# Kernel tuning notes

Hardware: AMD Instinct MI355X
Metric: run time of the kernel (lower is better)

Reference implementation:

```python
import jax, jax.numpy as jnp
import numpy as np

N_NODES = 100000
N_EDGES = 3200000
F_IN = 256
HEADS = 8
C_OUT = 8
NEG_SLOPE = 0.2


def setup_inputs() -> dict:
    key = jax.random.key(0)
    k1, k2, k3, k4, k5, k6 = jax.random.split(key, 6)
    x = jax.random.normal(k1, (N_NODES, F_IN), dtype=jnp.float32)
    edge_index = jax.random.randint(k2, (2, N_EDGES), 0, N_NODES, dtype=jnp.int64)
    W = jax.random.normal(k3, (F_IN, HEADS * C_OUT), dtype=jnp.float32) * (1.0 / np.sqrt(F_IN))
    att_src = jax.random.normal(k4, (HEADS, C_OUT), dtype=jnp.float32) * 0.1
    att_dst = jax.random.normal(k5, (HEADS, C_OUT), dtype=jnp.float32) * 0.1
    bias = jax.random.normal(k6, (HEADS * C_OUT,), dtype=jnp.float32) * 0.01
    return {"x": x, "edge_index": edge_index, "W": W, "att_src": att_src, "att_dst": att_dst, "bias": bias}


def reference(x, edge_index, W, att_src, att_dst, bias):
    # GATConv (PyG semantics), concat=True, inference (dropout off).
    N = x.shape[0]
    H, C = att_src.shape
    h = (x @ W).reshape(N, H, C)                      # [N,H,C] transformed features
    a_src = jnp.einsum('nhc,hc->nh', h, att_src)      # [N,H]
    a_dst = jnp.einsum('nhc,hc->nh', h, att_dst)      # [N,H]
    src, dst = edge_index[0], edge_index[1]
    # per-edge raw attention logits
    e = jax.nn.leaky_relu(a_src[src] + a_dst[dst], NEG_SLOPE)  # [E,H]
    # segment softmax over incoming edges of each destination node
    m = jax.ops.segment_max(e, dst, num_segments=N)            # [N,H]
    e = jnp.exp(e - m[dst])
    s = jax.ops.segment_sum(e, dst, num_segments=N)            # [N,H]
    alpha = e / (s[dst] + 1e-16)                               # [E,H]
    # scatter-add weighted neighbor features
    out = jax.ops.segment_sum(alpha[:, :, None] * h[src], dst, num_segments=N)  # [N,H,C]
    return out.reshape(N, H * C) + bias
```

## Files before the change

### kernel.cpp

```cpp
#include <hip/hip_runtime.h>
#include <hip/hip_fp16.h>
#include <math.h>

#define F_IN 256
#define HC 64
#define NHEAD 8
#define NEG 0.2f
#define BSH 7
#define BSZ 128
#define CAP 5376
#define HCAP 2944

typedef __attribute__((ext_vector_type(8))) short bf16x8;
typedef __attribute__((ext_vector_type(4))) float f32x4;

union BV { uint4 q; bf16x8 v; };

__device__ __forceinline__ unsigned int hi_pair(float a, float b) {
  return __builtin_amdgcn_perm(__float_as_uint(a), __float_as_uint(b), 0x03020706u);
}
__device__ __forceinline__ unsigned int lo_pair(float a, float b) {
  float ra = a - __uint_as_float(__float_as_uint(a) & 0xffff0000u);
  float rb = b - __uint_as_float(__float_as_uint(b) & 0xffff0000u);
  return __builtin_amdgcn_perm(__float_as_uint(ra), __float_as_uint(rb), 0x03020706u);
}

__global__ __launch_bounds__(256) void k_prep(const float* __restrict__ W,
                                              unsigned short* __restrict__ Wp,
                                              int* __restrict__ bcursor, int NB) {
  int b = blockIdx.x, t = threadIdx.x;
  if (b >= 64) {
    int i = (b - 64) * 256 + t;
    if (i < NB) bcursor[i] = 0;
    return;
  }
  int idx = b * 256 + t;
  int k = idx >> 6, c = idx & 63;
  float w = W[idx];
  unsigned int u = __float_as_uint(w);
  unsigned short hi = (unsigned short)((u + 0x7fffu + ((u >> 16) & 1u)) >> 16);
  float r = w - __uint_as_float((unsigned int)hi << 16);
  unsigned int ur = __float_as_uint(r);
  unsigned short lo = (unsigned short)((ur + 0x7fffu + ((ur >> 16) & 1u)) >> 16);
  int ks = k >> 5, j = k & 7, lg = (k >> 3) & 3;
  int lane = lg * 16 + (c & 15), cg = c >> 4;
  int off = ((ks * 4 + cg) * 64 + lane) * 8 + j;
  Wp[off] = hi;
  Wp[16384 + off] = lo;
}

__global__ __launch_bounds__(512, 4) void k_fused(
    const float* __restrict__ x, const uint4* __restrict__ Wp4,
    const float* __restrict__ att_src, const float* __restrict__ att_dst,
    __half2* __restrict__ h2, float* __restrict__ asrc, float* __restrict__ adst,
    const int* __restrict__ edge, int* __restrict__ bcursor,
    unsigned int* __restrict__ entries, int N, int E, int NB, int NG, int NP) {
  __shared__ unsigned long long srt8[8192];
  __shared__ int hist[1024];
  __shared__ int loff[1024];
  __shared__ int basearr[1024];
  __shared__ int pr[512];
  int b = blockIdx.x;
  int mn = min(NG, NP), m2 = 2 * mn;
  int type, idx;
  if (b < m2) { type = b & 1; idx = b >> 1; }
  else { type = (NG > NP) ? 0 : 1; idx = mn + (b - m2); }
  int t = threadIdx.x;

  if (type == 0) {
    int wv = t >> 6, l = t & 63;
    int lr = l & 15, lg = l >> 4;
    int r0 = idx * 256 + wv * 32;
    int ra = r0 + lr;      if (ra > N - 1) ra = N - 1;
    int rb = r0 + 16 + lr; if (rb > N - 1) rb = N - 1;
    const float* xr0 = x + (size_t)ra * F_IN + lg * 8;
    const float* xr1 = x + (size_t)rb * F_IN + lg * 8;
    const uint4* wp = Wp4 + l;

    float as4[4], ad4[4];
#pragma unroll
    for (int cg = 0; cg < 4; cg++) {
      as4[cg] = att_src[cg * 16 + lr];
      ad4[cg] = att_dst[cg * 16 + lr];
    }

    f32x4 acc[2][4];
#pragma unroll
    for (int i = 0; i < 2; i++)
#pragma unroll
      for (int j = 0; j < 4; j++) acc[i][j] = (f32x4){0.f, 0.f, 0.f, 0.f};

#pragma unroll
    for (int ks = 0; ks < 8; ks++) {
      float4 p0 = *(const float4*)(xr0 + ks * 32);
      float4 q0 = *(const float4*)(xr0 + ks * 32 + 4);
      float4 p1 = *(const float4*)(xr1 + ks * 32);
      float4 q1 = *(const float4*)(xr1 + ks * 32 + 4);
      BV bh[4], bl[4];
#pragma unroll
      for (int cg = 0; cg < 4; cg++) {
        bh[cg].q = wp[(ks * 4 + cg) * 64];
        bl[cg].q = wp[2048 + (ks * 4 + cg) * 64];
      }
      BV ah0, al0, ah1, al1;
      ah0.q.x = hi_pair(p0.x, p0.y); ah0.q.y = hi_pair(p0.z, p0.w);
      ah0.q.z = hi_pair(q0.x, q0.y); ah0.q.w = hi_pair(q0.z, q0.w);
      al0.q.x = lo_pair(p0.x, p0.y); al0.q.y = lo_pair(p0.z, p0.w);
      al0.q.z = lo_pair(q0.x, q0.y); al0.q.w = lo_pair(q0.z, q0.w);
      ah1.q.x = hi_pair(p1.x, p1.y); ah1.q.y = hi_pair(p1.z, p1.w);
      ah1.q.z = hi_pair(q1.x, q1.y); ah1.q.w = hi_pair(q1.z, q1.w);
      al1.q.x = lo_pair(p1.x, p1.y); al1.q.y = lo_pair(p1.z, p1.w);
      al1.q.z = lo_pair(q1.x, q1.y); al1.q.w = lo_pair(q1.z, q1.w);
#pragma unroll
      for (int cg = 0; cg < 4; cg++) {
        acc[0][cg] = __builtin_amdgcn_mfma_f32_16x16x32_bf16(ah0.v, bh[cg].v, acc[0][cg], 0, 0, 0);
        acc[0][cg] = __builtin_amdgcn_mfma_f32_16x16x32_bf16(al0.v, bh[cg].v, acc[0][cg], 0, 0, 0);
        acc[0][cg] = __builtin_amdgcn_mfma_f32_16x16x32_bf16(ah0.v, bl[cg].v, acc[0][cg], 0, 0, 0);
        acc[1][cg] = __builtin_amdgcn_mfma_f32_16x16x32_bf16(ah1.v, bh[cg].v, acc[1][cg], 0, 0, 0);
        acc[1][cg] = __builtin_amdgcn_mfma_f32_16x16x32_bf16(al1.v, bh[cg].v, acc[1][cg], 0, 0, 0);
        acc[1][cg] = __builtin_amdgcn_mfma_f32_16x16x32_bf16(ah1.v, bl[cg].v, acc[1][cg], 0, 0, 0);
      }
    }

#pragma unroll
    for (int rg = 0; rg < 2; rg++) {
#pragma unroll
      for (int tt = 0; tt < 4; tt++) {
        int node = r0 + rg * 16 + 4 * lg + tt;
        bool ok = node < N;
        float v0 = acc[rg][0][tt], v1 = acc[rg][1][tt], v2 = acc[rg][2][tt], v3 = acc[rg][3][tt];
        float o0 = __shfl_xor(v0, 1), o1 = __shfl_xor(v1, 1);
        float o2 = __shfl_xor(v2, 1), o3 = __shfl_xor(v3, 1);
        if (ok && !(l & 1)) {
          size_t hb = (size_t)node * 32 + (lr >> 1);
          h2[hb]      = __halves2half2(__float2half_rn(v0), __float2half_rn(o0));
          h2[hb + 8]  = __halves2half2(__float2half_rn(v1), __float2half_rn(o1));
          h2[hb + 16] = __halves2half2(__float2half_rn(v2), __float2half_rn(o2));
          h2[hb + 24] = __halves2half2(__float2half_rn(v3), __float2half_rn(o3));
        }
#pragma unroll
        for (int cg = 0; cg < 4; cg++) {
          float v = (cg == 0) ? v0 : (cg == 1) ? v1 : (cg == 2) ? v2 : v3;
          float s = v * as4[cg];
          float d = v * ad4[cg];
          s += __shfl_xor(s, 1); d += __shfl_xor(d, 1);
          s += __shfl_xor(s, 2); d += __shfl_xor(d, 2);
          s += __shfl_xor(s, 4); d += __shfl_xor(d, 4);
          if (ok && !(l & 7)) {
            int hd = 2 * cg + (lr >> 3);
            asrc[node * NHEAD + hd] = s;
            adst[node * NHEAD + hd] = d;
          }
        }
      }
    }
    return;
  }

  int base = idx * 8192;
  int cblk = min(8192, E - base);
  for (int i = t; i < 1024; i += 512) hist[i] = 0;
  __syncthreads();
#pragma unroll
  for (int j = 0; j < 16; j++) {
    int e = base + j * 512 + t;
    if (e < E) atomicAdd(&hist[edge[E + e] >> BSH], 1);
  }
  __syncthreads();
  int a = hist[2 * t], bb = hist[2 * t + 1];
  pr[t] = a + bb;
  __syncthreads();
  for (int off = 1; off < 512; off <<= 1) {
    int add = (t >= off) ? pr[t - off] : 0;
    __syncthreads();
    pr[t] += add;
    __syncthreads();
  }
  int excl = pr[t] - (a + bb);
  loff[2 * t] = excl;
  loff[2 * t + 1] = excl + a;
  if (a > 0 && 2 * t < NB) basearr[2 * t] = atomicAdd(&bcursor[2 * t], a);
  if (bb > 0 && 2 * t + 1 < NB) basearr[2 * t + 1] = atomicAdd(&bcursor[2 * t + 1], bb);
  hist[2 * t] = excl;
  hist[2 * t + 1] = excl + a;
  __syncthreads();
#pragma unroll
  for (int j = 0; j < 16; j++) {
    int e = base + j * 512 + t;
    if (e < E) {
      int s = edge[e], d = edge[E + e];
      int p = atomicAdd(&hist[d >> BSH], 1);
      srt8[p] = ((unsigned long long)(unsigned int)d << 32) | (unsigned int)s;
    }
  }
  __syncthreads();
  for (int i = t; i < cblk; i += 512) {
    unsigned long long v = srt8[i];
    int d = (int)(v >> 32), s = (int)(v & 0xFFFFFFFFu);
    int bk = d >> BSH;
    int local = basearr[bk] + (i - loff[bk]);
    if (local < CAP)
      entries[(size_t)bk * CAP + local] = ((unsigned int)(d & (BSZ - 1)) << 17) | (unsigned int)s;
  }
}

__global__ __launch_bounds__(512, 6) void k_bagg(
    const unsigned int* __restrict__ entries, const int* __restrict__ bcursor,
    const __half2* __restrict__ h2, const float* __restrict__ asrc,
    const float* __restrict__ adst, const float* __restrict__ bias,
    float* __restrict__ out, int N) {
  __shared__ int srt[HCAP];
  __shared__ int hist[64];
  __shared__ int cur[64];
  __shared__ int off[65];
  __shared__ int tmp[64];
  int t = threadIdx.x;
  int bkt = blockIdx.x >> 1;
  int hf = blockIdx.x & 1;
  int n0 = (bkt << BSH) + (hf << 6);
  int ncnt = min(64, N - n0);
  if (ncnt <= 0) return;
  int cnt = bcursor[bkt];
  if (cnt > CAP) cnt = CAP;
  const unsigned int* ebase = entries + (size_t)bkt * CAP;
  if (t < 64) hist[t] = 0;
  __syncthreads();
  for (int i = t; i < cnt; i += 512) {
    int d = (int)(ebase[i] >> 17);
    if ((d >> 6) == hf) atomicAdd(&hist[d & 63], 1);
  }
  __syncthreads();
  if (t < 64) tmp[t] = hist[t];
  __syncthreads();
  for (int o = 1; o < 64; o <<= 1) {
    int add = (t < 64 && t >= o) ? tmp[t - o] : 0;
    __syncthreads();
    if (t < 64) tmp[t] += add;
    __syncthreads();
  }
  if (t < 64) { off[t] = tmp[t] - hist[t]; cur[t] = tmp[t] - hist[t]; }
  if (t == 63) off[64] = tmp[63];
  __syncthreads();
  for (int i = t; i < cnt; i += 512) {
    unsigned int v = ebase[i];
    int d = (int)(v >> 17);
    if ((d >> 6) == hf) {
      int p = atomicAdd(&cur[d & 63], 1);
      if (p < HCAP) srt[p] = (int)(v & 0x1FFFF);
    }
  }
  __syncthreads();
  int wv = t >> 6, l = t & 63;
  int eslot = l >> 3, cg = l & 7;
  for (int nd = wv; nd < ncnt; nd += 8) {
    int node = n0 + nd;
    int sbeg = min(off[nd], HCAP), send = min(off[nd + 1], HCAP);
    float ad = adst[node * NHEAD + cg];
    float a0 = 0.f, a1 = 0.f, a2 = 0.f, a3 = 0.f;
    float a4 = 0.f, a5 = 0.f, a6 = 0.f, a7 = 0.f;
    float wsum = 0.f;
    for (int k = sbeg; k < send; k += 8) {
      int idx = k + eslot;
      bool val = idx < send;
      int s = srt[val ? idx : send - 1];
      float lg = asrc[s * NHEAD + cg] + ad;
      float w = __expf(fmaxf(lg, NEG * lg));
      w = val ? w : 0.f;
      union { uint4 q; __half2 h[4]; } u;
      u.q = *((const uint4*)(h2 + (size_t)s * 32) + cg);
      float2 f0 = __half22float2(u.h[0]);
      float2 f1 = __half22float2(u.h[1]);
      float2 f2 = __half22float2(u.h[2]);
      float2 f3 = __half22float2(u.h[3]);
      a0 = fmaf(w, f0.x, a0); a1 = fmaf(w, f0.y, a1);
      a2 = fmaf(w, f1.x, a2); a3 = fmaf(w, f1.y, a3);
      a4 = fmaf(w, f2.x, a4); a5 = fmaf(w, f2.y, a5);
      a6 = fmaf(w, f3.x, a6); a7 = fmaf(w, f3.y, a7);
      wsum += w;
    }
#pragma unroll
    for (int m = 8; m < 64; m <<= 1) {
      a0 += __shfl_xor(a0, m); a1 += __shfl_xor(a1, m);
      a2 += __shfl_xor(a2, m); a3 += __shfl_xor(a3, m);
      a4 += __shfl_xor(a4, m); a5 += __shfl_xor(a5, m);
      a6 += __shfl_xor(a6, m); a7 += __shfl_xor(a7, m);
      wsum += __shfl_xor(wsum, m);
    }
    if (l < 8) {
      float inv = wsum > 0.f ? 1.0f / wsum : 0.f;
      float4 b0 = *(const float4*)&bias[cg * 8];
      float4 b1 = *(const float4*)&bias[cg * 8 + 4];
      float4 r0, r1;
      r0.x = fmaf(a0, inv, b0.x); r0.y = fmaf(a1, inv, b0.y);
      r0.z = fmaf(a2, inv, b0.z); r0.w = fmaf(a3, inv, b0.w);
      r1.x = fmaf(a4, inv, b1.x); r1.y = fmaf(a5, inv, b1.y);
      r1.z = fmaf(a6, inv, b1.z); r1.w = fmaf(a7, inv, b1.w);
      *(float4*)&out[(size_t)node * HC + cg * 8] = r0;
      *(float4*)&out[(size_t)node * HC + cg * 8 + 4] = r1;
    }
  }
}

extern "C" void kernel_launch(void* const* d_in, const int* in_sizes, int n_in,
                              void* d_out, int out_size, void* d_ws, size_t ws_size,
                              hipStream_t stream) {
  const float* x = (const float*)d_in[0];
  const int* edge = (const int*)d_in[1];
  const float* W = (const float*)d_in[2];
  const float* att_src = (const float*)d_in[3];
  const float* att_dst = (const float*)d_in[4];
  const float* bias = (const float*)d_in[5];
  int N = in_sizes[0] / F_IN;
  int E = in_sizes[1] / 2;
  float* out = (float*)d_out;
  int NB = (N + BSZ - 1) >> BSH;

  unsigned short* Wp = (unsigned short*)d_ws;
  __half2* h2 = (__half2*)((char*)d_ws + 65536);
  float* asrc = (float*)(h2 + (size_t)N * 32);
  float* adst = asrc + (size_t)N * NHEAD;
  int* bcursor = (int*)(adst + (size_t)N * NHEAD);
  unsigned int* entries = (unsigned int*)(bcursor + ((NB + 3) & ~3));

  int NG = (N + 255) / 256;
  int NP = (E + 8191) / 8192;
  int nzb = (NB + 255) / 256;

  k_prep<<<64 + nzb, 256, 0, stream>>>(W, Wp, bcursor, NB);
  k_fused<<<NG + NP, 512, 0, stream>>>(x, (const uint4*)Wp, att_src, att_dst,
                                       h2, asrc, adst, edge, bcursor, entries,
                                       N, E, NB, NG, NP);
  k_bagg<<<2 * NB, 512, 0, stream>>>(entries, bcursor, h2, asrc, adst, bias, out, N);
}
```

Measured before the change: 322.7 us.

## Stage x tiles into LDS via async global_load_lds with double buffering

After: 307.6 us. 1.05x faster.

```diff
diff --git a/kernel.cpp b/kernel.cpp
--- a/kernel.cpp
+++ b/kernel.cpp
@@ -55,7 +55,7 @@
     __half2* __restrict__ h2, float* __restrict__ asrc, float* __restrict__ adst,
     const int* __restrict__ edge, int* __restrict__ bcursor,
     unsigned int* __restrict__ entries, int N, int E, int NB, int NG, int NP) {
-  __shared__ unsigned long long srt8[8192];
+  __shared__ __align__(16) unsigned long long srt8[8192];
   __shared__ int hist[1024];
   __shared__ int loff[1024];
   __shared__ int basearr[1024];
@@ -70,12 +70,8 @@
   if (type == 0) {
     int wv = t >> 6, l = t & 63;
     int lr = l & 15, lg = l >> 4;
-    int r0 = idx * 256 + wv * 32;
-    int ra = r0 + lr;      if (ra > N - 1) ra = N - 1;
-    int rb = r0 + 16 + lr; if (rb > N - 1) rb = N - 1;
-    const float* xr0 = x + (size_t)ra * F_IN + lg * 8;
-    const float* xr1 = x + (size_t)rb * F_IN + lg * 8;
-    const uint4* wp = Wp4 + l;
+    int r0blk = idx * 256;
+    char* xb = (char*)srt8;
 
     float as4[4], ad4[4];
 #pragma unroll
@@ -83,6 +79,7 @@
       as4[cg] = att_src[cg * 16 + lr];
       ad4[cg] = att_dst[cg * 16 + lr];
     }
+    const uint4* wp = Wp4 + l;
 
     f32x4 acc[2][4];
 #pragma unroll
@@ -90,12 +87,37 @@
 #pragma unroll
       for (int j = 0; j < 4; j++) acc[i][j] = (f32x4){0.f, 0.f, 0.f, 0.f};
 
+#define STAGE(ks_, buf_)                                                        \
+    {                                                                           \
+      _Pragma("unroll")                                                         \
+      for (int rd = 0; rd < 4; rd++) {                                          \
+        int Lbase = rd * 512 + wv * 64;                                         \
+        int L = Lbase + l;                                                      \
+        int r_ = L >> 3;                                                        \
+        int g_ = (L & 7) ^ (r_ & 7);                                            \
+        int grow = r0blk + r_; if (grow > N - 1) grow = N - 1;                  \
+        __builtin_amdgcn_global_load_lds(                                       \
+            (const void*)(x + (size_t)grow * F_IN + (ks_) * 32 + g_ * 4),       \
+            (void*)(xb + (buf_) * 32768 + (size_t)Lbase * 16), 16, 0, 0);       \
+      }                                                                         \
+    }
+
+    STAGE(0, 0);
+    int ra_t = wv * 32 + lr, rb_t = ra_t + 16;
+    int s0 = ra_t * 8 + ((lg * 2 + 0) ^ (ra_t & 7));
+    int s1 = ra_t * 8 + ((lg * 2 + 1) ^ (ra_t & 7));
+    int s2 = rb_t * 8 + ((lg * 2 + 0) ^ (rb_t & 7));
+    int s3 = rb_t * 8 + ((lg * 2 + 1) ^ (rb_t & 7));
+
 #pragma unroll
     for (int ks = 0; ks < 8; ks++) {
-      float4 p0 = *(const float4*)(xr0 + ks * 32);
-      float4 q0 = *(const float4*)(xr0 + ks * 32 + 4);
-      float4 p1 = *(const float4*)(xr1 + ks * 32);
-      float4 q1 = *(const float4*)(xr1 + ks * 32 + 4);
+      if (ks < 7) STAGE(ks + 1, (ks + 1) & 1);
+      __syncthreads();
+      const char* cb = xb + (ks & 1) * 32768;
+      float4 p0 = *(const float4*)(cb + (size_t)s0 * 16);
+      float4 q0 = *(const float4*)(cb + (size_t)s1 * 16);
+      float4 p1 = *(const float4*)(cb + (size_t)s2 * 16);
+      float4 q1 = *(const float4*)(cb + (size_t)s3 * 16);
       BV bh[4], bl[4];
 #pragma unroll
       for (int cg = 0; cg < 4; cg++) {
@@ -120,8 +142,11 @@
         acc[1][cg] = __builtin_amdgcn_mfma_f32_16x16x32_bf16(al1.v, bh[cg].v, acc[1][cg], 0, 0, 0);
         acc[1][cg] = __builtin_amdgcn_mfma_f32_16x16x32_bf16(ah1.v, bl[cg].v, acc[1][cg], 0, 0, 0);
       }
-    }
-
+      __syncthreads();
+    }
+#undef STAGE
+
+    int r0 = r0blk + wv * 32;
 #pragma unroll
     for (int rg = 0; rg < 2; rg++) {
 #pragma unroll
```
